# Performance work log

Hardware: AMD Instinct MI355X
Metric: run time of the kernel (lower is better)

## Reference

```python
import jax, jax.numpy as jnp
import numpy as np

B, N, C, M, OUT = 4, 256, 32, 4, 64


def _uniform(k, shape, fan_in):
    s = 1.0 / np.sqrt(fan_in)
    return jax.random.uniform(k, shape, jnp.float32, -s, s)


def setup_inputs() -> dict:
    key = jax.random.key(0)
    ks = jax.random.split(key, 11)
    return {
        "x": jax.random.normal(ks[0], (B, N, N, C), jnp.float32),
        # Neighborhood / SnConv2to1 linears (in=C, out=M neighborhood channels)
        "w1_nb": _uniform(ks[1], (3 * C, M), 3 * C),
        "b1_nb": _uniform(ks[2], (M,), 3 * C),
        "w0_nb": _uniform(ks[3], (2 * C, M), 2 * C),
        "b0_nb": _uniform(ks[4], (M,), 2 * C),
        # SnConv2 linears (in channels = M*C after neighborhood product)
        "w2d": _uniform(ks[5], (2 * M * C, OUT), 2 * M * C),
        "b2d": _uniform(ks[6], (OUT,), 2 * M * C),
        "w1d": _uniform(ks[7], (3 * M * C, OUT), 3 * M * C),
        "b1d": _uniform(ks[8], (OUT,), 3 * M * C),
        "w0d": _uniform(ks[9], (2 * M * C, OUT), 2 * M * C),
        "b0d": _uniform(ks[10], (OUT,), 2 * M * C),
    }


def _contractions(x):
    # x: [B, n, n, c]; mask=None, reduction='mean' path of _get_contractions
    n = x.shape[1]
    rowsum = x.sum(axis=1) / n                      # [B, n, c]
    colsum = x.sum(axis=2) / n                      # [B, n, c]
    diag = jnp.diagonal(x, axis1=1, axis2=2)        # [B, c, n]
    rowcolsum = x.sum(axis=(1, 2)) / (n * n)        # [B, c]
    diag_sum = diag.sum(axis=-1) / n                # [B, c]  (/= sqrt(n^2))
    diag = jnp.moveaxis(diag, -1, 1)                # move_from_end -> [B, n, c]
    return rowsum, colsum, diag, rowcolsum, diag_sum


def reference(x, w1_nb, b1_nb, w0_nb, b0_nb, w2d, b2d, w1d, b1d, w0d, b0d):
    # ---- Neighborhood: SnConv2to1 -> sigmoid ----
    rs, cs, dg, rcs, ds = _contractions(x)
    obj1 = jnp.concatenate([rs, cs, dg], axis=-1)             # [B, n, 3C]
    obj0 = jnp.concatenate([rcs, ds], axis=-1)                # [B, 2C]
    node = obj1 @ w1_nb + b1_nb + (obj0 @ w0_nb + b0_nb)[:, None, :]
    neighbs = jax.nn.sigmoid(node)                            # [B, n, M]
    # ---- _neighbor_elementwise_product ----
    expanded = neighbs[:, None, :, :] * neighbs[:, :, None, :]  # [B, n, n, M]
    # channel_product: outer product over channel dims, collapsed to M*C
    xl = (expanded[..., :, None] * x[..., None, :]).reshape(B, N, N, M * C)
    # ---- SnConv2 on the localized tensor ----
    rs2, cs2, dg2, rcs2, ds2 = _contractions(xl)
    obj2d = jnp.concatenate([xl, jnp.swapaxes(xl, 1, 2)], axis=-1)  # [B,n,n,2MC]
    obj1d = jnp.concatenate([rs2, cs2, dg2], axis=-1)               # [B,n,3MC]
    obj0d = jnp.concatenate([rcs2, ds2], axis=-1)                   # [B,2MC]
    out = (obj2d @ w2d + b2d
           + (obj1d @ w1d + b1d)[:, None, :, :]
           + (obj0d @ w0d + b0d)[:, None, None, :])                 # [B,n,n,OUT]
    return out
```

## Files before the change

kernel.cpp:

```cpp
#include <hip/hip_runtime.h>
#include <math.h>

#define Bv 4
#define Nv 256
#define Cv 32
#define Mv 4
#define OUTv 64
#define MCv (Mv*Cv)

typedef _Float16 h8 __attribute__((ext_vector_type(8)));
typedef _Float16 h4 __attribute__((ext_vector_type(4)));
typedef float f4 __attribute__((ext_vector_type(4)));

__device__ __align__(16) float g_rs  [Bv * Nv * Cv];
__device__ __align__(16) float g_cs  [Bv * Nv * Cv];
__device__ __align__(16) float g_dgx [Bv * Nv * Cv];
__device__ __align__(16) float g_nb  [Bv * Nv * Mv];
__device__ __align__(16) float g_rcs2R[8 * Bv * MCv];
__device__ __align__(16) float g_ds2R [8 * Bv * MCv];
__device__ __align__(16) float g_addv[Bv * Nv * OUTv];
__device__ __align__(16) _Float16 g_wfrag[8 * 4 * 64 * 8];

__global__ __launch_bounds__(256) void k_contract1(const float* __restrict__ x,
                                                   const float* __restrict__ w2d) {
    int bx = blockIdx.x, b = blockIdx.y;
    int t = threadIdx.x;
    if (bx >= 2 * Nv) {
        if (b != 0) return;
        int r = bx - 2 * Nv;
        if (r == 8) {
            float4 z = {0.f,0.f,0.f,0.f};
            #pragma unroll
            for (int k = 0; k < 4; k++) {
                ((float4*)g_rcs2R)[k * 256 + t] = z;
                ((float4*)g_ds2R )[k * 256 + t] = z;
            }
            return;
        }
        int fi = r * 256 + t;
        int s = fi >> 8, q = (fi >> 6) & 3, lane = fi & 63;
        int k0 = s * 32 + ((lane >> 4) << 3);
        int o = q * 16 + (lane & 15);
        #pragma unroll
        for (int jj = 0; jj < 8; jj++)
            g_wfrag[fi * 8 + jj] = (_Float16)w2d[(size_t)(k0 + jj) * OUTv + o];
        return;
    }
    int c4 = t & 7, sub = t >> 3;
    const float4* xb4 = (const float4*)(x + (size_t)b * Nv * Nv * Cv);
    __shared__ float red[32][36];
    float4 acc = {0.f,0.f,0.f,0.f};
    if (bx < Nv) {
        int n = bx;
        for (int i = sub; i < Nv; i += 32) {
            float4 v = xb4[((size_t)i * Nv + n) * 8 + c4];
            acc.x += v.x; acc.y += v.y; acc.z += v.z; acc.w += v.w;
        }
        red[sub][c4*4+0] = acc.x; red[sub][c4*4+1] = acc.y;
        red[sub][c4*4+2] = acc.z; red[sub][c4*4+3] = acc.w;
        __syncthreads();
        if (t < 32) {
            float s = 0.f;
            #pragma unroll
            for (int k = 0; k < 32; k++) s += red[k][t];
            g_rs[(b * Nv + n) * Cv + t] = s * (1.0f / Nv);
        }
        if (t < 8) ((float4*)g_dgx)[(b * Nv + n) * 8 + t] = xb4[((size_t)n * Nv + n) * 8 + t];
    } else {
        int n = bx - Nv;
        for (int j = sub; j < Nv; j += 32) {
            float4 v = xb4[((size_t)n * Nv + j) * 8 + c4];
            acc.x += v.x; acc.y += v.y; acc.z += v.z; acc.w += v.w;
        }
        red[sub][c4*4+0] = acc.x; red[sub][c4*4+1] = acc.y;
        red[sub][c4*4+2] = acc.z; red[sub][c4*4+3] = acc.w;
        __syncthreads();
        if (t < 32) {
            float s = 0.f;
            #pragma unroll
            for (int k = 0; k < 32; k++) s += red[k][t];
            g_cs[(b * Nv + n) * Cv + t] = s * (1.0f / Nv);
        }
    }
}

__global__ __launch_bounds__(256) void k_fused(const float* __restrict__ x,
    const float* __restrict__ w1, const float* __restrict__ b1,
    const float* __restrict__ w0, const float* __restrict__ b0,
    const float* __restrict__ w1d, const float* __restrict__ b1d,
    const float* __restrict__ b2d, const float* __restrict__ b0d) {
    int n = blockIdx.x, b = blockIdx.y;
    int t = threadIdx.x;

    __shared__ float red8[8][64];
    __shared__ float obj0[64];
    __shared__ float t0nb[4];
    __shared__ __align__(16) float nb4[Nv][4];
    __shared__ float red[32][132];
    __shared__ float S1l[MCv], S2l[MCv];
    __shared__ float redD[4][64];

    {
        int c = t & 31, sub = t >> 5;
        float ar = 0.f, ad = 0.f;
        for (int nn = sub; nn < Nv; nn += 8) {
            ar += g_rs[(b * Nv + nn) * Cv + c];
            ad += g_dgx[(b * Nv + nn) * Cv + c];
        }
        red8[sub][c] = ar;
        red8[sub][32 + c] = ad;
    }
    __syncthreads();
    if (t < 64) {
        float s = 0.f;
        #pragma unroll
        for (int k = 0; k < 8; k++) s += red8[k][t];
        obj0[t] = s * (1.0f / Nv);
    }
    __syncthreads();
    if (t < 4) {
        float v = b0[t];
        for (int k = 0; k < 2 * Cv; k++) v += obj0[k] * w0[k * Mv + t];
        t0nb[t] = v;
    }
    __syncthreads();
    {
        const float4* rs4 = (const float4*)(g_rs  + (size_t)(b * Nv + t) * Cv);
        const float4* cs4 = (const float4*)(g_cs  + (size_t)(b * Nv + t) * Cv);
        const float4* dg4 = (const float4*)(g_dgx + (size_t)(b * Nv + t) * Cv);
        float node[4];
        #pragma unroll
        for (int m = 0; m < 4; m++) node[m] = t0nb[m] + b1[m];
        #pragma unroll
        for (int q = 0; q < 8; q++) {
            float4 R = rs4[q], S = cs4[q], D = dg4[q];
            #pragma unroll
            for (int e = 0; e < 4; e++) {
                int cc = q * 4 + e;
                float r = ((const float*)&R)[e];
                float s = ((const float*)&S)[e];
                float d = ((const float*)&D)[e];
                #pragma unroll
                for (int m = 0; m < 4; m++)
                    node[m] += r * w1[cc * Mv + m] + s * w1[(Cv + cc) * Mv + m]
                             + d * w1[(2 * Cv + cc) * Mv + m];
            }
        }
        float4 nv;
        #pragma unroll
        for (int m = 0; m < 4; m++)
            ((float*)&nv)[m] = 1.0f / (1.0f + expf(-node[m]));
        *(float4*)nb4[t] = nv;
        if (n == 0) ((float4*)g_nb)[b * Nv + t] = nv;
    }
    __syncthreads();

    const float4* xb4 = (const float4*)(x + (size_t)b * Nv * Nv * Cv);
    int c4 = t & 7, sub3 = t >> 3;

    {
        float4 a[4];
        #pragma unroll
        for (int m = 0; m < 4; m++) a[m] = {0.f,0.f,0.f,0.f};
        for (int i = sub3; i < Nv; i += 32) {
            float4 v = xb4[((size_t)i * Nv + n) * 8 + c4];
            float4 nv = *(const float4*)nb4[i];
            a[0].x += nv.x*v.x; a[0].y += nv.x*v.y; a[0].z += nv.x*v.z; a[0].w += nv.x*v.w;
            a[1].x += nv.y*v.x; a[1].y += nv.y*v.y; a[1].z += nv.y*v.z; a[1].w += nv.y*v.w;
            a[2].x += nv.z*v.x; a[2].y += nv.z*v.y; a[2].z += nv.z*v.z; a[2].w += nv.z*v.w;
            a[3].x += nv.w*v.x; a[3].y += nv.w*v.y; a[3].z += nv.w*v.z; a[3].w += nv.w*v.w;
        }
        #pragma unroll
        for (int m = 0; m < 4; m++) {
            red[sub3][m*32 + c4*4+0] = a[m].x; red[sub3][m*32 + c4*4+1] = a[m].y;
            red[sub3][m*32 + c4*4+2] = a[m].z; red[sub3][m*32 + c4*4+3] = a[m].w;
        }
    }
    __syncthreads();
    if (t < 128) {
        float s = 0.f;
        #pragma unroll
        for (int k = 0; k < 32; k++) s += red[k][t];
        S1l[t] = s;
        int m = t >> 5, c = t & 31;
        float nv = nb4[n][m];
        int rep = ((n & 7) * Bv + b) * MCv + t;
        atomicAdd(&g_rcs2R[rep], nv * s);
        atomicAdd(&g_ds2R [rep], nv * nv * g_dgx[(b * Nv + n) * Cv + c]);
    }
    __syncthreads();

    {
        float4 a[4];
        #pragma unroll
        for (int m = 0; m < 4; m++) a[m] = {0.f,0.f,0.f,0.f};
        for (int j = sub3; j < Nv; j += 32) {
            float4 v = xb4[((size_t)n * Nv + j) * 8 + c4];
            float4 nv = *(const float4*)nb4[j];
            a[0].x += nv.x*v.x; a[0].y += nv.x*v.y; a[0].z += nv.x*v.z; a[0].w += nv.x*v.w;
            a[1].x += nv.y*v.x; a[1].y += nv.y*v.y; a[1].z += nv.y*v.z; a[1].w += nv.y*v.w;
            a[2].x += nv.z*v.x; a[2].y += nv.z*v.y; a[2].z += nv.z*v.z; a[2].w += nv.z*v.w;
            a[3].x += nv.w*v.x; a[3].y += nv.w*v.y; a[3].z += nv.w*v.z; a[3].w += nv.w*v.w;
        }
        #pragma unroll
        for (int m = 0; m < 4; m++) {
            red[sub3][m*32 + c4*4+0] = a[m].x; red[sub3][m*32 + c4*4+1] = a[m].y;
            red[sub3][m*32 + c4*4+2] = a[m].z; red[sub3][m*32 + c4*4+3] = a[m].w;
        }
    }
    __syncthreads();
    if (t < 128) {
        float s = 0.f;
        #pragma unroll
        for (int k = 0; k < 32; k++) s += red[k][t];
        S2l[t] = s;
    }
    __syncthreads();

    {
        int o = t & 63, ks = t >> 6;
        const float invN = 1.0f / Nv;
        float nv = nb4[n][ks];
        float f = nv * invN, d2 = nv * nv;
        const float* dgr = g_dgx + (size_t)(b * Nv + n) * Cv;
        float acc = 0.f;
        #pragma unroll 8
        for (int cc = 0; cc < 32; cc++) {
            int mc = ks * 32 + cc;
            acc += f * S1l[mc] * w1d[(size_t)mc * OUTv + o]
                 + f * S2l[mc] * w1d[(size_t)(MCv + mc) * OUTv + o]
                 + d2 * dgr[cc] * w1d[(size_t)(2 * MCv + mc) * OUTv + o];
        }
        redD[ks][o] = acc;
    }
    __syncthreads();
    if (t < 64) {
        float v = redD[0][t] + redD[1][t] + redD[2][t] + redD[3][t]
                + b1d[t] + b2d[t] + b0d[t];
        g_addv[(size_t)(b * Nv + n) * OUTv + t] = v;
    }
}

#define XPAD 40
__global__ __launch_bounds__(256) void k_main(const float* __restrict__ x,
                                              float* __restrict__ out,
                                              const float* __restrict__ w0d) {
    int jt = blockIdx.x, ip = blockIdx.y, b = blockIdx.z;
    int i0 = ip * 2, i1 = i0 + 1;
    int j0 = jt * 128;
    int t = threadIdx.x;
    int lane = t & 63, w = t >> 6;
    int rowA = lane & 15, quad = lane >> 4;

    __shared__ __align__(16) _Float16 Wl[8 * 4 * 64 * 8];
    __shared__ __align__(16) _Float16 Xt0[128 * XPAD];
    __shared__ __align__(16) _Float16 Xb0[128 * XPAD];
    __shared__ __align__(16) _Float16 Xt1[128 * XPAD];
    __shared__ __align__(16) _Float16 Xb1[128 * XPAD];
    __shared__ float rcl[MCv], dsl[MCv];
    __shared__ float t0red[4][64];
    __shared__ float t0l[64];

    {
        const float4* src = (const float4*)g_wfrag;
        float4* dst = (float4*)Wl;
        #pragma unroll
        for (int r = 0; r < 8; r++) dst[r * 256 + t] = src[r * 256 + t];
    }
    {
        const float4* x4 = (const float4*)x;
        #pragma unroll
        for (int r = 0; r < 4; r++) {
            int idx = r * 256 + t;
            int j = idx >> 3, c4 = idx & 7;
            float4 v0 = x4[((size_t)(b * Nv + i0) * Nv + j0 + j) * 8 + c4];
            float4 v1 = x4[((size_t)(b * Nv + i1) * Nv + j0 + j) * 8 + c4];
            float4 u0 = x4[((size_t)(b * Nv + j0 + j) * Nv + i0) * 8 + c4];
            float4 u1 = x4[((size_t)(b * Nv + j0 + j) * Nv + i1) * 8 + c4];
            h4 h0; h0[0] = (_Float16)v0.x; h0[1] = (_Float16)v0.y;
            h0[2] = (_Float16)v0.z; h0[3] = (_Float16)v0.w;
            *(h4*)&Xt0[j * XPAD + c4 * 4] = h0;
            h4 h1; h1[0] = (_Float16)v1.x; h1[1] = (_Float16)v1.y;
            h1[2] = (_Float16)v1.z; h1[3] = (_Float16)v1.w;
            *(h4*)&Xt1[j * XPAD + c4 * 4] = h1;
            h4 g0; g0[0] = (_Float16)u0.x; g0[1] = (_Float16)u0.y;
            g0[2] = (_Float16)u0.z; g0[3] = (_Float16)u0.w;
            *(h4*)&Xb0[j * XPAD + c4 * 4] = g0;
            h4 g1; g1[0] = (_Float16)u1.x; g1[1] = (_Float16)u1.y;
            g1[2] = (_Float16)u1.z; g1[3] = (_Float16)u1.w;
            *(h4*)&Xb1[j * XPAD + c4 * 4] = g1;
        }
    }
    if (t < 128) {
        float s = 0.f;
        #pragma unroll
        for (int r = 0; r < 8; r++) s += g_rcs2R[(r * Bv + b) * MCv + t];
        rcl[t] = s;
    } else {
        int tt = t - 128;
        float s = 0.f;
        #pragma unroll
        for (int r = 0; r < 8; r++) s += g_ds2R[(r * Bv + b) * MCv + tt];
        dsl[tt] = s;
    }
    int jl1 = w * 32 + rowA, jl2 = jl1 + 16;
    _Float16 e1h0[4], e2h0[4], e1h1[4], e2h1[4];
    {
        const float* ni0 = g_nb + (size_t)(b * Nv + i0) * Mv;
        const float* ni1 = g_nb + (size_t)(b * Nv + i1) * Mv;
        const float* n1 = g_nb + (size_t)(b * Nv + j0 + jl1) * Mv;
        const float* n2 = g_nb + (size_t)(b * Nv + j0 + jl2) * Mv;
        #pragma unroll
        for (int m = 0; m < 4; m++) {
            e1h0[m] = (_Float16)(ni0[m] * n1[m]);
            e2h0[m] = (_Float16)(ni0[m] * n2[m]);
            e1h1[m] = (_Float16)(ni1[m] * n1[m]);
            e2h1[m] = (_Float16)(ni1[m] * n2[m]);
        }
    }
    __syncthreads();
    {
        int o = t & 63, ks = t >> 6;
        const float invN = 1.0f / Nv;
        const float invN2 = invN * invN;
        float a0 = 0.f;
        #pragma unroll 8
        for (int cc = 0; cc < 32; cc++) {
            int mc = ks * 32 + cc;
            a0 += invN2 * rcl[mc] * w0d[(size_t)mc * OUTv + o]
                + invN  * dsl[mc] * w0d[(size_t)(MCv + mc) * OUTv + o];
        }
        t0red[ks][o] = a0;
    }
    __syncthreads();
    if (t < 64) t0l[t] = t0red[0][t] + t0red[1][t] + t0red[2][t] + t0red[3][t];
    __syncthreads();

    f4 acc[2][2][4];
    #pragma unroll
    for (int ii = 0; ii < 2; ii++)
        #pragma unroll
        for (int js = 0; js < 2; js++)
            #pragma unroll
            for (int q = 0; q < 4; q++) acc[ii][js][q] = {0.f, 0.f, 0.f, 0.f};

    const h8* Wf = (const h8*)Wl;
    #pragma unroll
    for (int part = 0; part < 2; part++) {
        const _Float16* X0 = part ? Xb0 : Xt0;
        const _Float16* X1 = part ? Xb1 : Xt1;
        h8 xv1_0 = *(const h8*)&X0[jl1 * XPAD + quad * 8];
        h8 xv2_0 = *(const h8*)&X0[jl2 * XPAD + quad * 8];
        h8 xv1_1 = *(const h8*)&X1[jl1 * XPAD + quad * 8];
        h8 xv2_1 = *(const h8*)&X1[jl2 * XPAD + quad * 8];
        #pragma unroll
        for (int m = 0; m < 4; m++) {
            h8 a1_0 = xv1_0 * e1h0[m];
            h8 a2_0 = xv2_0 * e2h0[m];
            h8 a1_1 = xv1_1 * e1h1[m];
            h8 a2_1 = xv2_1 * e2h1[m];
            int s = part * 4 + m;
            #pragma unroll
            for (int q = 0; q < 4; q++) {
                h8 bf = Wf[(s * 4 + q) * 64 + lane];
                acc[0][0][q] = __builtin_amdgcn_mfma_f32_16x16x32_f16(a1_0, bf, acc[0][0][q], 0, 0, 0);
                acc[0][1][q] = __builtin_amdgcn_mfma_f32_16x16x32_f16(a2_0, bf, acc[0][1][q], 0, 0, 0);
                acc[1][0][q] = __builtin_amdgcn_mfma_f32_16x16x32_f16(a1_1, bf, acc[1][0][q], 0, 0, 0);
                acc[1][1][q] = __builtin_amdgcn_mfma_f32_16x16x32_f16(a2_1, bf, acc[1][1][q], 0, 0, 0);
            }
        }
    }
    #pragma unroll
    for (int js = 0; js < 2; js++) {
        int jbase = j0 + w * 32 + js * 16 + quad * 4;
        #pragma unroll
        for (int q = 0; q < 4; q++) {
            int o = q * 16 + rowA;
            float tv = t0l[o];
            #pragma unroll
            for (int r = 0; r < 4; r++) {
                int j = jbase + r;
                float av = g_addv[(size_t)(b * Nv + j) * OUTv + o] + tv;
                out[(((size_t)(b * Nv + i0)) * Nv + j) * OUTv + o] = acc[0][js][q][r] + av;
                out[(((size_t)(b * Nv + i1)) * Nv + j) * OUTv + o] = acc[1][js][q][r] + av;
            }
        }
    }
}

extern "C" void kernel_launch(void* const* d_in, const int* in_sizes, int n_in,
                              void* d_out, int out_size, void* d_ws, size_t ws_size,
                              hipStream_t stream) {
    const float* x     = (const float*)d_in[0];
    const float* w1_nb = (const float*)d_in[1];
    const float* b1_nb = (const float*)d_in[2];
    const float* w0_nb = (const float*)d_in[3];
    const float* b0_nb = (const float*)d_in[4];
    const float* w2d   = (const float*)d_in[5];
    const float* b2d   = (const float*)d_in[6];
    const float* w1d   = (const float*)d_in[7];
    const float* b1d   = (const float*)d_in[8];
    const float* w0d   = (const float*)d_in[9];
    const float* b0d   = (const float*)d_in[10];
    float* out = (float*)d_out;
    (void)d_ws; (void)ws_size;

    hipLaunchKernelGGL(k_contract1, dim3(2 * Nv + 9, Bv), dim3(256), 0, stream, x, w2d);
    hipLaunchKernelGGL(k_fused, dim3(Nv, Bv), dim3(256), 0, stream,
                       x, w1_nb, b1_nb, w0_nb, b0_nb, w1d, b1d, b2d, b0d);
    hipLaunchKernelGGL(k_main, dim3(2, Nv / 2, Bv), dim3(256), 0, stream, x, out, w0d);
}
```

Measured before the change: 171.8 us.

## Add explicit transpose pass so strided column reads become contiguous

Adds a kernel that writes a transposed copy of x (swapping the two spatial axes) into a global buffer through shared memory. The column-sum, weighted column-sum and the transposed tile loads in the main kernel then read this copy contiguously instead of gathering rows with a large stride. In exchange it adds an extra full read and write of the 32 MB input plus one more launch, which may cost more than the strided-access penalty saves.

```diff
diff --git a/kernel.cpp b/kernel.cpp
--- a/kernel.cpp
+++ b/kernel.cpp
@@ -12,6 +12,7 @@
 typedef _Float16 h4 __attribute__((ext_vector_type(4)));
 typedef float f4 __attribute__((ext_vector_type(4)));
 
+__device__ __align__(16) float g_xT  [Bv * Nv * Nv * Cv];
 __device__ __align__(16) float g_rs  [Bv * Nv * Cv];
 __device__ __align__(16) float g_cs  [Bv * Nv * Cv];
 __device__ __align__(16) float g_dgx [Bv * Nv * Cv];
@@ -20,6 +21,27 @@
 __device__ __align__(16) float g_ds2R [8 * Bv * MCv];
 __device__ __align__(16) float g_addv[Bv * Nv * OUTv];
 __device__ __align__(16) _Float16 g_wfrag[8 * 4 * 64 * 8];
+
+__global__ __launch_bounds__(256) void k_transpose(const float* __restrict__ x) {
+    int it = blockIdx.x, jt = blockIdx.y, b = blockIdx.z;
+    int i0 = it * 8, j0 = jt * 32;
+    int t = threadIdx.x;
+    __shared__ __align__(16) float4 T[32 * 65];
+    const float4* x4  = (const float4*)(x    + (size_t)b * Nv * Nv * Cv);
+    float4*       xT4 = (float4*)      (g_xT + (size_t)b * Nv * Nv * Cv);
+    #pragma unroll
+    for (int r = 0; r < 8; r++) {
+        int j = t >> 3, c4 = t & 7;
+        T[j * 65 + r * 8 + c4] = x4[((size_t)(i0 + r) * Nv + j0 + j) * 8 + c4];
+    }
+    __syncthreads();
+    #pragma unroll
+    for (int r = 0; r < 8; r++) {
+        int idx = r * 256 + t;
+        int j = idx >> 6, i = (idx >> 3) & 7, c4 = idx & 7;
+        xT4[((size_t)(j0 + j) * Nv + i0 + i) * 8 + c4] = T[j * 65 + i * 8 + c4];
+    }
+}
 
 __global__ __launch_bounds__(256) void k_contract1(const float* __restrict__ x,
                                                    const float* __restrict__ w2d) {
@@ -47,13 +69,13 @@
         return;
     }
     int c4 = t & 7, sub = t >> 3;
-    const float4* xb4 = (const float4*)(x + (size_t)b * Nv * Nv * Cv);
     __shared__ float red[32][36];
     float4 acc = {0.f,0.f,0.f,0.f};
     if (bx < Nv) {
         int n = bx;
+        const float4* xT4 = (const float4*)(g_xT + (size_t)b * Nv * Nv * Cv);
         for (int i = sub; i < Nv; i += 32) {
-            float4 v = xb4[((size_t)i * Nv + n) * 8 + c4];
+            float4 v = xT4[((size_t)n * Nv + i) * 8 + c4];
             acc.x += v.x; acc.y += v.y; acc.z += v.z; acc.w += v.w;
         }
         red[sub][c4*4+0] = acc.x; red[sub][c4*4+1] = acc.y;
@@ -65,9 +87,13 @@
             for (int k = 0; k < 32; k++) s += red[k][t];
             g_rs[(b * Nv + n) * Cv + t] = s * (1.0f / Nv);
         }
-        if (t < 8) ((float4*)g_dgx)[(b * Nv + n) * 8 + t] = xb4[((size_t)n * Nv + n) * 8 + t];
+        if (t < 8) {
+            const float4* xb4 = (const float4*)(x + (size_t)b * Nv * Nv * Cv);
+            ((float4*)g_dgx)[(b * Nv + n) * 8 + t] = xb4[((size_t)n * Nv + n) * 8 + t];
+        }
     } else {
         int n = bx - Nv;
+        const float4* xb4 = (const float4*)(x + (size_t)b * Nv * Nv * Cv);
         for (int j = sub; j < Nv; j += 32) {
             float4 v = xb4[((size_t)n * Nv + j) * 8 + c4];
             acc.x += v.x; acc.y += v.y; acc.z += v.z; acc.w += v.w;
@@ -155,7 +181,8 @@
     }
     __syncthreads();
 
-    const float4* xb4 = (const float4*)(x + (size_t)b * Nv * Nv * Cv);
+    const float4* xb4  = (const float4*)(x    + (size_t)b * Nv * Nv * Cv);
+    const float4* xT4b = (const float4*)(g_xT + (size_t)b * Nv * Nv * Cv);
     int c4 = t & 7, sub3 = t >> 3;
 
     {
@@ -163,7 +190,7 @@
         #pragma unroll
         for (int m = 0; m < 4; m++) a[m] = {0.f,0.f,0.f,0.f};
         for (int i = sub3; i < Nv; i += 32) {
-            float4 v = xb4[((size_t)i * Nv + n) * 8 + c4];
+            float4 v = xT4b[((size_t)n * Nv + i) * 8 + c4];
             float4 nv = *(const float4*)nb4[i];
             a[0].x += nv.x*v.x; a[0].y += nv.x*v.y; a[0].z += nv.x*v.z; a[0].w += nv.x*v.w;
             a[1].x += nv.y*v.x; a[1].y += nv.y*v.y; a[1].z += nv.y*v.z; a[1].w += nv.y*v.w;
@@ -268,15 +295,16 @@
         for (int r = 0; r < 8; r++) dst[r * 256 + t] = src[r * 256 + t];
     }
     {
-        const float4* x4 = (const float4*)x;
+        const float4* x4  = (const float4*)x;
+        const float4* xT4 = (const float4*)g_xT;
         #pragma unroll
         for (int r = 0; r < 4; r++) {
             int idx = r * 256 + t;
             int j = idx >> 3, c4 = idx & 7;
-            float4 v0 = x4[((size_t)(b * Nv + i0) * Nv + j0 + j) * 8 + c4];
-            float4 v1 = x4[((size_t)(b * Nv + i1) * Nv + j0 + j) * 8 + c4];
-            float4 u0 = x4[((size_t)(b * Nv + j0 + j) * Nv + i0) * 8 + c4];
-            float4 u1 = x4[((size_t)(b * Nv + j0 + j) * Nv + i1) * 8 + c4];
+            float4 v0 = x4 [((size_t)(b * Nv + i0) * Nv + j0 + j) * 8 + c4];
+            float4 v1 = x4 [((size_t)(b * Nv + i1) * Nv + j0 + j) * 8 + c4];
+            float4 u0 = xT4[((size_t)(b * Nv + i0) * Nv + j0 + j) * 8 + c4];
+            float4 u1 = xT4[((size_t)(b * Nv + i1) * Nv + j0 + j) * 8 + c4];
             h4 h0; h0[0] = (_Float16)v0.x; h0[1] = (_Float16)v0.y;
             h0[2] = (_Float16)v0.z; h0[3] = (_Float16)v0.w;
             *(h4*)&Xt0[j * XPAD + c4 * 4] = h0;
@@ -405,6 +433,7 @@
     float* out = (float*)d_out;
     (void)d_ws; (void)ws_size;
 
+    hipLaunchKernelGGL(k_transpose, dim3(Nv / 8, Nv / 32, Bv), dim3(256), 0, stream, x);
     hipLaunchKernelGGL(k_contract1, dim3(2 * Nv + 9, Bv), dim3(256), 0, stream, x, w2d);
     hipLaunchKernelGGL(k_fused, dim3(Nv, Bv), dim3(256), 0, stream,
                        x, w1_nb, b1_nb, w0_nb, b0_nb, w1d, b1d, b2d, b0d);
```

Measured after the change: 182.1 us. 1.06x slower.
